# Kernel optimization log

Hardware: AMD Instinct MI355X
Metric: run time of the kernel (lower is better)

Reference implementation:

```python
import jax, jax.numpy as jnp
from jax import lax
import numpy as np

B, T, C, W = 128, 64, 64, 27
H, K = 128, 3
EPS = 1e-5


def _conv1d(x, w, b):
    # x: (N, Cin, W), w: (Cout, Cin, K) -> (N, Cout, W), 'same' padding
    y = lax.conv_general_dilated(x, w, (1,), 'SAME', dimension_numbers=('NCH', 'OIH', 'NCH'))
    return y + b[None, :, None]


def _mish(x):
    return x * jnp.tanh(jax.nn.softplus(x))


def _gru_layer(x_seq, act_seq, gw, gb, cw, cb, aw, ab, bn_g, bn_b):
    # x_seq: (T, B, Cin, W); act_seq: (T, B, 8, W)
    Hd = bn_g.shape[0]

    def step(h, xa):
        x, a = xa
        gates = _conv1d(jnp.concatenate([x, h], axis=1), gw, gb)  # (B, 2H, W)
        reset = jax.nn.sigmoid(gates[:, :Hd])
        update = jax.nn.sigmoid(gates[:, Hd:])
        cnm = _conv1d(jnp.concatenate([x, reset * h], axis=1), cw, cb) + _conv1d(a, aw, ab)
        pre = _mish((1.0 - update) * h + update * cnm)
        # BatchNorm1d (training mode): per-channel stats over (batch, width)
        mean = pre.mean(axis=(0, 2), keepdims=True)
        var = pre.var(axis=(0, 2), keepdims=True)
        h_next = bn_g[None, :, None] * (pre - mean) * lax.rsqrt(var + EPS) + bn_b[None, :, None]
        return h_next, h_next

    h0 = jnp.zeros((x_seq.shape[1], Hd, x_seq.shape[3]), dtype=x_seq.dtype)
    _, ys = lax.scan(step, h0, (x_seq, act_seq))
    return ys  # (T, B, H, W)


def setup_inputs():
    key = jax.random.key(0)
    ks = jax.random.split(key, 16)
    s = 0.05
    d = {}
    d['input_tensor'] = jax.random.normal(ks[0], (B, T, C, W), dtype=jnp.float32)
    # layer 0 (cur_input_dim = C)
    d['gates_w0'] = jax.random.normal(ks[1], (2 * H, C + H, K)) * s
    d['gates_b0'] = jnp.zeros((2 * H,))
    d['can_w0'] = jax.random.normal(ks[2], (H, C + H, K)) * s
    d['can_b0'] = jnp.zeros((H,))
    d['cond_w0'] = jax.random.normal(ks[3], (H, 8, K)) * s
    d['cond_b0'] = jnp.zeros((H,))
    d['bn_g0'] = jnp.ones((H,))
    d['bn_b0'] = jnp.zeros((H,))
    # layer 1 (cur_input_dim = H)
    d['gates_w1'] = jax.random.normal(ks[4], (2 * H, H + H, K)) * s
    d['gates_b1'] = jnp.zeros((2 * H,))
    d['can_w1'] = jax.random.normal(ks[5], (H, H + H, K)) * s
    d['can_b1'] = jnp.zeros((H,))
    d['cond_w1'] = jax.random.normal(ks[6], (H, 8, K)) * s
    d['cond_b1'] = jnp.zeros((H,))
    d['bn_g1'] = jnp.ones((H,))
    d['bn_b1'] = jnp.zeros((H,))
    # concentrate linear: (27*H) -> 1
    d['conc_w'] = jax.random.normal(ks[7], (1, W * H)) * s
    d['conc_b'] = jnp.zeros((1,))
    return d


def reference(input_tensor, gates_w0, gates_b0, can_w0, can_b0, cond_w0, cond_b0, bn_g0, bn_b0,
              gates_w1, gates_b1, can_w1, can_b1, cond_w1, cond_b1, bn_g1, bn_b1, conc_w, conc_b):
    x_t = jnp.transpose(input_tensor, (1, 0, 2, 3))  # (T, B, C, W)
    act_t = x_t[:, :, -8:, :]                        # (T, B, 8, W)
    h1 = _gru_layer(x_t, act_t, gates_w0, gates_b0, can_w0, can_b0, cond_w0, cond_b0, bn_g0, bn_b0)
    h2 = _gru_layer(h1, act_t, gates_w1, gates_b1, can_w1, can_b1, cond_w1, cond_b1, bn_g1, bn_b1)
    # (T, B, H, W) -> (B, T, H*W)
    out = jnp.transpose(h2, (1, 0, 2, 3)).reshape(input_tensor.shape[0], input_tensor.shape[1], -1)
    reward = out @ conc_w.T[:, 0] + conc_b[0]        # (B, T)
    return 0.99 * (reward[:, -1] - reward[:, -2])
```

## Files before the change

kernel.cpp:

```cpp
#include <hip/hip_runtime.h>
#include <math.h>

#define Bn 128
#define Tn 64
#define Cn 64
#define Wn 27
#define Hn 128
#define EPSf 1e-5f
#define NBWf 3456.0f

struct Params {
  const float* in;
  const float* wt_g0; const float* gb0;
  const float* wt_c0; const float* cb0;
  const float* wt_a0; const float* ab0;
  const float* bg0; const float* bb0;
  const float* wt_g1; const float* gb1;
  const float* wt_c1; const float* cb1;
  const float* wt_a1; const float* ab1;
  const float* bg1; const float* bb1;
  const float* concw;
  float* pre1a; float* pre1b; float* pre2a; float* pre2b;
  float* sums;
  unsigned* cnt;
  float* out;
};

__device__ __forceinline__ void bn_coef(const float* __restrict__ sums,
                                        const float* __restrict__ g,
                                        const float* __restrict__ b,
                                        int c, float& sc, float& sh) {
  float s1 = sums[2 * c], s2 = sums[2 * c + 1];
  float mean = s1 * (1.0f / NBWf);
  float var = s2 * (1.0f / NBWf) - mean * mean;
  sc = g[c] * rsqrtf(var + EPSf);
  sh = b[c] - mean * sc;
}

__device__ __forceinline__ float sigm(float x) {
  return 1.0f / (1.0f + __expf(-x));
}

__device__ __forceinline__ int swz(int row, int c) {
  return row * 32 + ((((c >> 2) ^ (row & 7)) & 7) << 2) + (c & 3);
}

__device__ __forceinline__ void conv_row(const float* __restrict__ rowbase,
                                         int sw, float w0, float w1, float w2,
                                         float* __restrict__ acc) {
  const float4* rp = (const float4*)rowbase;
  float xa[16];
  {
    float4 v0 = rp[0 ^ sw];
    float4 v1 = rp[1 ^ sw];
    float4 v2 = rp[2 ^ sw];
    float4 v3 = rp[3 ^ sw];
    xa[0] = v0.x; xa[1] = v0.y; xa[2] = v0.z; xa[3] = v0.w;
    xa[4] = v1.x; xa[5] = v1.y; xa[6] = v1.z; xa[7] = v1.w;
    xa[8] = v2.x; xa[9] = v2.y; xa[10] = v2.z; xa[11] = v2.w;
    xa[12] = v3.x; xa[13] = v3.y; xa[14] = v3.z; xa[15] = v3.w;
  }
#pragma unroll
  for (int c = 1; c <= 14; ++c)
    acc[c - 1] = fmaf(w2, xa[c + 1], fmaf(w1, xa[c], fmaf(w0, xa[c - 1], acc[c - 1])));
  float xc[15];
  xc[0] = xa[14]; xc[1] = xa[15];
  {
    float4 v4 = rp[4 ^ sw];
    float4 v5 = rp[5 ^ sw];
    float4 v6 = rp[6 ^ sw];
    float4 v7 = rp[7 ^ sw];
    xc[2] = v4.x; xc[3] = v4.y; xc[4] = v4.z; xc[5] = v4.w;
    xc[6] = v5.x; xc[7] = v5.y; xc[8] = v5.z; xc[9] = v5.w;
    xc[10] = v6.x; xc[11] = v6.y; xc[12] = v6.z; xc[13] = v6.w;
    xc[14] = v7.x;
  }
#pragma unroll
  for (int k = 0; k < 13; ++k)
    acc[14 + k] = fmaf(w2, xc[k + 2], fmaf(w1, xc[k + 1], fmaf(w0, xc[k], acc[14 + k])));
}

template <int IC, bool XN>
__device__ void step_body(const Params& p, int b, int t, bool hv,
    const float* __restrict__ xpre, const float* __restrict__ xs,
    const float* __restrict__ xg, const float* __restrict__ xb,
    const float* __restrict__ hpre, const float* __restrict__ hs,
    const float* __restrict__ hg, const float* __restrict__ hb,
    const float* __restrict__ wtg, const float* __restrict__ gbias,
    const float* __restrict__ wtc, const float* __restrict__ cbias,
    const float* __restrict__ wta, const float* __restrict__ abias,
    float* __restrict__ pre_out, float* __restrict__ sums_out,
    float* lx, float* lrh, float* lu) {
  const int tid = threadIdx.x;
  constexpr int ROWS = IC + 136;
  for (int r = tid; r < ROWS; r += 1024) {
    float sc = 1.f, sh = 0.f;
    const float* src = nullptr;
    if (r < IC) {
      if (XN) {
        bn_coef(xs, xg, xb, r, sc, sh);
        src = xpre + ((size_t)b * Hn + r) * Wn;
      } else {
        src = p.in + (((size_t)b * Tn + t) * Cn + r) * Wn;
      }
    } else if (r < IC + 128) {
      if (hv) {
        bn_coef(hs, hg, hb, r - IC, sc, sh);
        src = hpre + ((size_t)b * Hn + (r - IC)) * Wn;
      }
    } else {
      src = p.in + (((size_t)b * Tn + t) * Cn + 56 + (r - IC - 128)) * Wn;
    }
    lx[swz(r, 0)] = 0.f;
    lx[swz(r, 28)] = 0.f; lx[swz(r, 29)] = 0.f;
    lx[swz(r, 30)] = 0.f; lx[swz(r, 31)] = 0.f;
    if (src) {
      for (int w = 0; w < Wn; ++w) lx[swz(r, 1 + w)] = src[w] * sc + sh;
    } else {
      for (int w = 0; w < Wn; ++w) lx[swz(r, 1 + w)] = 0.f;
    }
  }
  __syncthreads();
  {
    const int rc = tid & 3;
    const int och = tid >> 2;
    float acc[27];
#pragma unroll
    for (int j = 0; j < 27; ++j) acc[j] = 0.f;
    const int rows = hv ? IC + 128 : IC;
    for (int i = rc; i < rows; i += 4) {
      const float* wp = wtg + (size_t)3 * i * 256 + och;
      float w0 = wp[0], w1 = wp[256], w2 = wp[512];
      conv_row(lx + i * 32, i & 7, w0, w1, w2, acc);
    }
#pragma unroll
    for (int j = 0; j < 27; ++j) {
      acc[j] += __shfl_xor(acc[j], 1);
      acc[j] += __shfl_xor(acc[j], 2);
    }
    if (rc == 0) {
      const float bias = gbias[och];
      if (och < 128) {
        lrh[swz(och, 0)] = 0.f;
        lrh[swz(och, 28)] = 0.f; lrh[swz(och, 29)] = 0.f;
        lrh[swz(och, 30)] = 0.f; lrh[swz(och, 31)] = 0.f;
#pragma unroll
        for (int c = 1; c <= 27; ++c) {
          float gv = sigm(acc[c - 1] + bias);
          lrh[swz(och, c)] = gv * lx[swz(IC + och, c)];
        }
      } else {
        const int ch = och - 128;
#pragma unroll
        for (int c = 1; c <= 27; ++c)
          lu[ch * 27 + (c - 1)] = sigm(acc[c - 1] + bias);
      }
    }
  }
  __syncthreads();
  {
    const int rc8 = tid & 7;
    const int ch = tid >> 3;
    float acc[27];
#pragma unroll
    for (int j = 0; j < 27; ++j) acc[j] = 0.f;
    for (int i = rc8; i < IC; i += 8) {
      const float* wp = wtc + (size_t)3 * i * 128 + ch;
      conv_row(lx + i * 32, i & 7, wp[0], wp[128], wp[256], acc);
    }
    if (hv) {
      for (int i = rc8; i < 128; i += 8) {
        const float* wp = wtc + (size_t)3 * (IC + i) * 128 + ch;
        conv_row(lrh + i * 32, i & 7, wp[0], wp[128], wp[256], acc);
      }
    }
    {
      const int i = rc8;
      const float* wp = wta + (size_t)3 * i * 128 + ch;
      const int r = IC + 128 + i;
      conv_row(lx + r * 32, r & 7, wp[0], wp[128], wp[256], acc);
    }
#pragma unroll
    for (int j = 0; j < 27; ++j) {
      acc[j] += __shfl_xor(acc[j], 1);
      acc[j] += __shfl_xor(acc[j], 2);
      acc[j] += __shfl_xor(acc[j], 4);
    }
    if (rc8 == 0) {
      const float cb = cbias[ch] + abias[ch];
      float s1 = 0.f, s2 = 0.f;
#pragma unroll
      for (int c = 1; c <= 27; ++c) {
        float u = lu[ch * 27 + (c - 1)];
        float hn = lx[swz(IC + ch, c)];
        float z = (1.f - u) * hn + u * (acc[c - 1] + cb);
        float pv;
        if (z > 20.f) {
          pv = z;
        } else {
          float q = 1.f + __expf(z);
          float q2 = q * q;
          pv = z * (q2 - 1.f) / (q2 + 1.f);
        }
        pre_out[((size_t)b * Hn + ch) * Wn + (c - 1)] = pv;
        s1 += pv;
        s2 += pv * pv;
      }
      atomicAdd(&sums_out[2 * ch], s1);
      atomicAdd(&sums_out[2 * ch + 1], s2);
    }
  }
}

__device__ __forceinline__ void gbar(unsigned* cnt, unsigned target) {
  __syncthreads();
  if (threadIdx.x == 0) {
    __threadfence();
    atomicAdd(cnt, 1u);
    while (__hip_atomic_load(cnt, __ATOMIC_RELAXED, __HIP_MEMORY_SCOPE_AGENT) < target) {
      __builtin_amdgcn_s_sleep(8);
    }
    __threadfence();
  }
  __syncthreads();
}

__global__ __launch_bounds__(1024, 4) void k_all(Params p) {
  __shared__ __align__(16) float lx[264 * 32];
  __shared__ __align__(16) float lrh[128 * 32];
  __shared__ float lu[128 * 27];
  const int bid = blockIdx.x;
  const bool L1b = bid >= 128;
  const int b = L1b ? bid - 128 : bid;
  float* pre1[2] = {p.pre1a, p.pre1b};
  float* pre2[2] = {p.pre2a, p.pre2b};
  for (int ph = 0; ph < 65; ++ph) {
    if (!L1b) {
      if (ph < 64) {
        const int t = ph;
        const bool hv = t > 0;
        step_body<Cn, false>(p, b, t, hv,
            nullptr, nullptr, nullptr, nullptr,
            hv ? pre1[(t - 1) & 1] : nullptr,
            hv ? p.sums + (size_t)(t - 1) * 256 : nullptr, p.bg0, p.bb0,
            p.wt_g0, p.gb0, p.wt_c0, p.cb0, p.wt_a0, p.ab0,
            pre1[t & 1], p.sums + (size_t)t * 256, lx, lrh, lu);
      }
    } else {
      if (ph >= 1) {
        const int t = ph - 1;
        const bool hv = t > 0;
        step_body<Hn, true>(p, b, t, hv,
            pre1[t & 1], p.sums + (size_t)t * 256, p.bg0, p.bb0,
            hv ? pre2[(t - 1) & 1] : nullptr,
            hv ? p.sums + (size_t)(64 + t - 1) * 256 : nullptr, p.bg1, p.bb1,
            p.wt_g1, p.gb1, p.wt_c1, p.cb1, p.wt_a1, p.ab1,
            pre2[t & 1], p.sums + (size_t)(64 + t) * 256, lx, lrh, lu);
      }
    }
    gbar(p.cnt, (unsigned)(ph + 1) * 256u);
  }
  if (!L1b) {
    const float* p63 = pre2[1];
    const float* p62 = pre2[0];
    const float* s63 = p.sums + (size_t)(64 + 63) * 256;
    const float* s62 = p.sums + (size_t)(64 + 62) * 256;
    const int tid = threadIdx.x;
    float acc = 0.f;
    for (int idx = tid; idx < Hn * Wn; idx += 1024) {
      int o = idx / Wn;
      float sc3, sh3, sc2, sh2;
      bn_coef(s63, p.bg1, p.bb1, o, sc3, sh3);
      bn_coef(s62, p.bg1, p.bb1, o, sc2, sh2);
      float v3 = p63[(size_t)b * Hn * Wn + idx] * sc3 + sh3;
      float v2 = p62[(size_t)b * Hn * Wn + idx] * sc2 + sh2;
      acc += (v3 - v2) * p.concw[idx];
    }
    lx[tid] = acc;
    __syncthreads();
    for (int s = 512; s > 0; s >>= 1) {
      if (tid < s) lx[tid] += lx[tid + s];
      __syncthreads();
    }
    if (tid == 0) p.out[b] = 0.99f * lx[0];
  }
}

__global__ void k_twt(const float* __restrict__ src, float* __restrict__ dst,
                      int M, int IC) {
  int idx = blockIdx.x * 256 + threadIdx.x;
  int total = M * IC * 3;
  if (idx >= total) return;
  int o = idx % M;
  int rem = idx / M;
  int i = rem / 3, k = rem - 3 * i;
  dst[idx] = src[((size_t)o * IC + i) * 3 + k];
}

extern "C" void kernel_launch(void* const* d_in, const int* in_sizes, int n_in,
                              void* d_out, int out_size, void* d_ws,
                              size_t ws_size, hipStream_t stream) {
  const float* in = (const float*)d_in[0];
  const float* gw0 = (const float*)d_in[1];
  const float* gb0 = (const float*)d_in[2];
  const float* cw0 = (const float*)d_in[3];
  const float* cb0 = (const float*)d_in[4];
  const float* aw0 = (const float*)d_in[5];
  const float* ab0 = (const float*)d_in[6];
  const float* bg0 = (const float*)d_in[7];
  const float* bb0 = (const float*)d_in[8];
  const float* gw1 = (const float*)d_in[9];
  const float* gb1 = (const float*)d_in[10];
  const float* cw1 = (const float*)d_in[11];
  const float* cb1 = (const float*)d_in[12];
  const float* aw1 = (const float*)d_in[13];
  const float* ab1 = (const float*)d_in[14];
  const float* bg1 = (const float*)d_in[15];
  const float* bb1 = (const float*)d_in[16];
  const float* concw = (const float*)d_in[17];
  float* out = (float*)d_out;

  float* ws = (float*)d_ws;
  size_t off = 0;
  float* wt_g0 = ws + off; off += 576 * 256;
  float* wt_c0 = ws + off; off += 576 * 128;
  float* wt_a0 = ws + off; off += 24 * 128;
  float* wt_g1 = ws + off; off += 768 * 256;
  float* wt_c1 = ws + off; off += 768 * 128;
  float* wt_a1 = ws + off; off += 24 * 128;
  const size_t PRE = (size_t)Bn * Hn * Wn;
  float* pre1a = ws + off; off += PRE;
  float* pre1b = ws + off; off += PRE;
  float* pre2a = ws + off; off += PRE;
  float* pre2b = ws + off; off += PRE;
  float* sums = ws + off; off += 2 * 64 * 256;
  unsigned* cnt = (unsigned*)(ws + off); off += 16;
  if (ws_size < off * sizeof(float)) return;

  hipMemsetAsync(sums, 0, (2 * 64 * 256 + 16) * sizeof(float), stream);

  auto tw = [&](const float* s, float* d, int M, int IC) {
    int tot = M * IC * 3;
    k_twt<<<(tot + 255) / 256, 256, 0, stream>>>(s, d, M, IC);
  };
  tw(gw0, wt_g0, 256, 192);
  tw(cw0, wt_c0, 128, 192);
  tw(aw0, wt_a0, 128, 8);
  tw(gw1, wt_g1, 256, 256);
  tw(cw1, wt_c1, 128, 256);
  tw(aw1, wt_a1, 128, 8);

  Params prm;
  prm.in = in;
  prm.wt_g0 = wt_g0; prm.gb0 = gb0;
  prm.wt_c0 = wt_c0; prm.cb0 = cb0;
  prm.wt_a0 = wt_a0; prm.ab0 = ab0;
  prm.bg0 = bg0; prm.bb0 = bb0;
  prm.wt_g1 = wt_g1; prm.gb1 = gb1;
  prm.wt_c1 = wt_c1; prm.cb1 = cb1;
  prm.wt_a1 = wt_a1; prm.ab1 = ab1;
  prm.bg1 = bg1; prm.bb1 = bb1;
  prm.concw = concw;
  prm.pre1a = pre1a; prm.pre1b = pre1b;
  prm.pre2a = pre2a; prm.pre2b = pre2b;
  prm.sums = sums; prm.cnt = cnt; prm.out = out;

  k_all<<<256, 1024, 0, stream>>>(prm);
}
```

Measured before the change: 7.402 ms.

## Pack conv weights as float4, parallelize row staging, use nontemporal loads/stores

Conv weights are re-laid out so the three taps for one (input, output) pair sit together in a padded float4, which turns three strided scalar loads into one 16-byte load. Row staging into shared memory now splits each row's 27 columns across 4 threads, so all 1024 threads take part instead of only one thread per row. Input loads and the pre-activation stores use nontemporal hints, and the launch-bounds occupancy hint drops from 4 to 2. The weight buffers grow by a third because of the padding, and the nontemporal hints could hurt reuse of the pre buffers, which are read again in the next step.

```diff
diff --git a/kernel.cpp b/kernel.cpp
--- a/kernel.cpp
+++ b/kernel.cpp
@@ -11,13 +11,13 @@
 
 struct Params {
   const float* in;
-  const float* wt_g0; const float* gb0;
-  const float* wt_c0; const float* cb0;
-  const float* wt_a0; const float* ab0;
+  const float4* wt_g0; const float* gb0;
+  const float4* wt_c0; const float* cb0;
+  const float4* wt_a0; const float* ab0;
   const float* bg0; const float* bb0;
-  const float* wt_g1; const float* gb1;
-  const float* wt_c1; const float* cb1;
-  const float* wt_a1; const float* ab1;
+  const float4* wt_g1; const float* gb1;
+  const float4* wt_c1; const float* cb1;
+  const float4* wt_a1; const float* ab1;
   const float* bg1; const float* bb1;
   const float* concw;
   float* pre1a; float* pre1b; float* pre2a; float* pre2b;
@@ -86,38 +86,48 @@
     const float* __restrict__ xg, const float* __restrict__ xb,
     const float* __restrict__ hpre, const float* __restrict__ hs,
     const float* __restrict__ hg, const float* __restrict__ hb,
-    const float* __restrict__ wtg, const float* __restrict__ gbias,
-    const float* __restrict__ wtc, const float* __restrict__ cbias,
-    const float* __restrict__ wta, const float* __restrict__ abias,
+    const float4* __restrict__ wtg, const float* __restrict__ gbias,
+    const float4* __restrict__ wtc, const float* __restrict__ cbias,
+    const float4* __restrict__ wta, const float* __restrict__ abias,
     float* __restrict__ pre_out, float* __restrict__ sums_out,
     float* lx, float* lrh, float* lu) {
   const int tid = threadIdx.x;
   constexpr int ROWS = IC + 136;
-  for (int r = tid; r < ROWS; r += 1024) {
-    float sc = 1.f, sh = 0.f;
-    const float* src = nullptr;
-    if (r < IC) {
-      if (XN) {
-        bn_coef(xs, xg, xb, r, sc, sh);
-        src = xpre + ((size_t)b * Hn + r) * Wn;
+  {
+    const int q = tid & 3;
+    const int w0c = q * 7;
+    const int wcnt = (q == 3) ? 6 : 7;
+    for (int r = tid >> 2; r < ROWS; r += 256) {
+      float sc = 1.f, sh = 0.f;
+      const float* src = nullptr;
+      if (r < IC) {
+        if (XN) {
+          bn_coef(xs, xg, xb, r, sc, sh);
+          src = xpre + ((size_t)b * Hn + r) * Wn;
+        } else {
+          src = p.in + (((size_t)b * Tn + t) * Cn + r) * Wn;
+        }
+      } else if (r < IC + 128) {
+        if (hv) {
+          bn_coef(hs, hg, hb, r - IC, sc, sh);
+          src = hpre + ((size_t)b * Hn + (r - IC)) * Wn;
+        }
       } else {
-        src = p.in + (((size_t)b * Tn + t) * Cn + r) * Wn;
-      }
-    } else if (r < IC + 128) {
-      if (hv) {
-        bn_coef(hs, hg, hb, r - IC, sc, sh);
-        src = hpre + ((size_t)b * Hn + (r - IC)) * Wn;
-      }
-    } else {
-      src = p.in + (((size_t)b * Tn + t) * Cn + 56 + (r - IC - 128)) * Wn;
-    }
-    lx[swz(r, 0)] = 0.f;
-    lx[swz(r, 28)] = 0.f; lx[swz(r, 29)] = 0.f;
-    lx[swz(r, 30)] = 0.f; lx[swz(r, 31)] = 0.f;
-    if (src) {
-      for (int w = 0; w < Wn; ++w) lx[swz(r, 1 + w)] = src[w] * sc + sh;
-    } else {
-      for (int w = 0; w < Wn; ++w) lx[swz(r, 1 + w)] = 0.f;
+        src = p.in + (((size_t)b * Tn + t) * Cn + 56 + (r - IC - 128)) * Wn;
+      }
+      if (q == 0) lx[swz(r, 0)] = 0.f;
+      if (q == 3) {
+        lx[swz(r, 28)] = 0.f; lx[swz(r, 29)] = 0.f;
+        lx[swz(r, 30)] = 0.f; lx[swz(r, 31)] = 0.f;
+      }
+      if (src) {
+        for (int j = 0; j < wcnt; ++j) {
+          float v = __builtin_nontemporal_load(src + w0c + j);
+          lx[swz(r, 1 + w0c + j)] = v * sc + sh;
+        }
+      } else {
+        for (int j = 0; j < wcnt; ++j) lx[swz(r, 1 + w0c + j)] = 0.f;
+      }
     }
   }
   __syncthreads();
@@ -129,9 +139,8 @@
     for (int j = 0; j < 27; ++j) acc[j] = 0.f;
     const int rows = hv ? IC + 128 : IC;
     for (int i = rc; i < rows; i += 4) {
-      const float* wp = wtg + (size_t)3 * i * 256 + och;
-      float w0 = wp[0], w1 = wp[256], w2 = wp[512];
-      conv_row(lx + i * 32, i & 7, w0, w1, w2, acc);
+      float4 w = wtg[i * 256 + och];
+      conv_row(lx + i * 32, i & 7, w.x, w.y, w.z, acc);
     }
 #pragma unroll
     for (int j = 0; j < 27; ++j) {
@@ -165,20 +174,20 @@
 #pragma unroll
     for (int j = 0; j < 27; ++j) acc[j] = 0.f;
     for (int i = rc8; i < IC; i += 8) {
-      const float* wp = wtc + (size_t)3 * i * 128 + ch;
-      conv_row(lx + i * 32, i & 7, wp[0], wp[128], wp[256], acc);
+      float4 w = wtc[i * 128 + ch];
+      conv_row(lx + i * 32, i & 7, w.x, w.y, w.z, acc);
     }
     if (hv) {
       for (int i = rc8; i < 128; i += 8) {
-        const float* wp = wtc + (size_t)3 * (IC + i) * 128 + ch;
-        conv_row(lrh + i * 32, i & 7, wp[0], wp[128], wp[256], acc);
+        float4 w = wtc[(IC + i) * 128 + ch];
+        conv_row(lrh + i * 32, i & 7, w.x, w.y, w.z, acc);
       }
     }
     {
       const int i = rc8;
-      const float* wp = wta + (size_t)3 * i * 128 + ch;
+      float4 w = wta[i * 128 + ch];
       const int r = IC + 128 + i;
-      conv_row(lx + r * 32, r & 7, wp[0], wp[128], wp[256], acc);
+      conv_row(lx + r * 32, r & 7, w.x, w.y, w.z, acc);
     }
 #pragma unroll
     for (int j = 0; j < 27; ++j) {
@@ -202,7 +211,8 @@
           float q2 = q * q;
           pv = z * (q2 - 1.f) / (q2 + 1.f);
         }
-        pre_out[((size_t)b * Hn + ch) * Wn + (c - 1)] = pv;
+        __builtin_nontemporal_store(pv,
+            pre_out + ((size_t)b * Hn + ch) * Wn + (c - 1));
         s1 += pv;
         s2 += pv * pv;
       }
@@ -225,7 +235,7 @@
   __syncthreads();
 }
 
-__global__ __launch_bounds__(1024, 4) void k_all(Params p) {
+__global__ __launch_bounds__(1024, 2) void k_all(Params p) {
   __shared__ __align__(16) float lx[264 * 32];
   __shared__ __align__(16) float lrh[128 * 32];
   __shared__ float lu[128 * 27];
@@ -286,15 +296,15 @@
   }
 }
 
-__global__ void k_twt(const float* __restrict__ src, float* __restrict__ dst,
-                      int M, int IC) {
+__global__ void k_twt4(const float* __restrict__ src, float4* __restrict__ dst,
+                       int M, int IC) {
   int idx = blockIdx.x * 256 + threadIdx.x;
-  int total = M * IC * 3;
+  int total = M * IC;
   if (idx >= total) return;
-  int o = idx % M;
-  int rem = idx / M;
-  int i = rem / 3, k = rem - 3 * i;
-  dst[idx] = src[((size_t)o * IC + i) * 3 + k];
+  int i = idx / M;
+  int o = idx - i * M;
+  const float* s = src + ((size_t)o * IC + i) * 3;
+  dst[idx] = make_float4(s[0], s[1], s[2], 0.f);
 }
 
 extern "C" void kernel_launch(void* const* d_in, const int* in_sizes, int n_in,
@@ -322,12 +332,12 @@
 
   float* ws = (float*)d_ws;
   size_t off = 0;
-  float* wt_g0 = ws + off; off += 576 * 256;
-  float* wt_c0 = ws + off; off += 576 * 128;
-  float* wt_a0 = ws + off; off += 24 * 128;
-  float* wt_g1 = ws + off; off += 768 * 256;
-  float* wt_c1 = ws + off; off += 768 * 128;
-  float* wt_a1 = ws + off; off += 24 * 128;
+  float4* wt_g0 = (float4*)(ws + off); off += 4 * 192 * 256;
+  float4* wt_c0 = (float4*)(ws + off); off += 4 * 192 * 128;
+  float4* wt_a0 = (float4*)(ws + off); off += 4 * 8 * 128;
+  float4* wt_g1 = (float4*)(ws + off); off += 4 * 256 * 256;
+  float4* wt_c1 = (float4*)(ws + off); off += 4 * 256 * 128;
+  float4* wt_a1 = (float4*)(ws + off); off += 4 * 8 * 128;
   const size_t PRE = (size_t)Bn * Hn * Wn;
   float* pre1a = ws + off; off += PRE;
   float* pre1b = ws + off; off += PRE;
@@ -339,9 +349,9 @@
 
   hipMemsetAsync(sums, 0, (2 * 64 * 256 + 16) * sizeof(float), stream);
 
-  auto tw = [&](const float* s, float* d, int M, int IC) {
-    int tot = M * IC * 3;
-    k_twt<<<(tot + 255) / 256, 256, 0, stream>>>(s, d, M, IC);
+  auto tw = [&](const float* s, float4* d, int M, int IC) {
+    int tot = M * IC;
+    k_twt4<<<(tot + 255) / 256, 256, 0, stream>>>(s, d, M, IC);
   };
   tw(gw0, wt_g0, 256, 192);
   tw(cw0, wt_c0, 128, 192);
```

New measurement: 8.393 ms. 13.4% more time.
